# Kernel optimization log

Hardware: AMD Instinct MI355X
Metric: run time of the kernel (lower is better)

## Reference

```python
import jax, jax.numpy as jnp
import numpy as np

H, F, E_SHARED, E_ROUTED, K = 1024, 4096, 1, 8, 2


def setup_inputs() -> dict:
    key = jax.random.key(0)
    ks = jax.random.split(key, 6)
    x = jax.random.normal(ks[0], (4, 2048, H), dtype=jnp.float32)
    s = 0.02
    shared_up = jax.random.normal(ks[1], (E_SHARED, H, F), dtype=jnp.float32) * s
    shared_down = jax.random.normal(ks[2], (E_SHARED, F, H), dtype=jnp.float32) * s
    routed_up = jax.random.normal(ks[3], (E_ROUTED, H, F), dtype=jnp.float32) * s
    routed_down = jax.random.normal(ks[4], (E_ROUTED, F, H), dtype=jnp.float32) * s
    router_w = jax.random.normal(ks[5], (H, E_ROUTED), dtype=jnp.float32) * s
    return {"x": x, "shared_up": shared_up, "shared_down": shared_down,
            "routed_up": routed_up, "routed_down": routed_down, "router_w": router_w}


def _expert(x, w_up, w_down):
    # ExpertBlock: down(gelu(up(x))), exact (erf) gelu as in torch F.gelu default
    h = jax.nn.gelu(jnp.einsum('bsh,hf->bsf', x, w_up), approximate=False)
    return jnp.einsum('bsf,fh->bsh', h, w_down)


def reference(x, shared_up, shared_down, routed_up, routed_down, router_w):
    # shared experts (always active)
    shared_out = jnp.zeros_like(x)
    for i in range(E_SHARED):
        shared_out = shared_out + _expert(x, shared_up[i], shared_down[i])

    # router: softmax over routed experts, then top-k gating
    probs = jax.nn.softmax(jnp.einsum('bsh,he->bse', x, router_w), axis=-1)
    top_k_prob, top_k_idx = jax.lax.top_k(probs, K)  # [B,S,K]
    # per-expert gate = sum of top-k probs assigned to that expert
    onehot = jax.nn.one_hot(top_k_idx, E_ROUTED, dtype=x.dtype)  # [B,S,K,E]
    gates = jnp.einsum('bsk,bske->bse', top_k_prob, onehot)      # [B,S,E]

    routed_out = jnp.zeros_like(x)
    for e in range(E_ROUTED):  # fixed small loop over experts
        y = _expert(x, routed_up[e], routed_down[e])
        routed_out = routed_out + gates[..., e:e + 1] * y

    return shared_out + routed_out + x
```

## Files before the change

kernel.cpp:

```cpp
#include <hip/hip_runtime.h>
#include <cstdint>
#include <cstddef>

#define HD 1024
#define FF 4096
#define TOK 8192
#define NSEG 9
#define ROWS_ROUTED (TOK*2)
#define ROWS_TOT (ROWS_ROUTED + TOK)

typedef __bf16 bf16;
typedef __bf16 bf16x8 __attribute__((ext_vector_type(8)));
typedef float  f32x4  __attribute__((ext_vector_type(4)));

__device__ __forceinline__ void stage16(const void* g, void* l) {
  __builtin_amdgcn_global_load_lds((const __attribute__((address_space(1))) void*)g,
                                   (__attribute__((address_space(3))) void*)l,
                                   16, 0, 0);
}

__device__ __forceinline__ unsigned short bf_bits(float v) {
  bf16 b = (bf16)v;
  return __builtin_bit_cast(unsigned short, b);
}

__global__ void k_init_meta(int* meta) {
  int t = threadIdx.x;
  if (t < 64) meta[t] = 0;
}

__global__ void k_convert_x(const float* __restrict__ x, bf16* __restrict__ xbf) {
  int i = blockIdx.x*256 + threadIdx.x;
  float4 v = reinterpret_cast<const float4*>(x)[i];
  ushort4 u;
  u.x = bf_bits(v.x); u.y = bf_bits(v.y); u.z = bf_bits(v.z); u.w = bf_bits(v.w);
  reinterpret_cast<ushort4*>(xbf)[i] = u;
}

__global__ void k_copy_out(const float* __restrict__ x, float* __restrict__ out) {
  int i = blockIdx.x*256 + threadIdx.x;
  reinterpret_cast<float4*>(out)[i] = reinterpret_cast<const float4*>(x)[i];
}

__global__ void k_tcvt(const float* __restrict__ routed, const float* __restrict__ shared_,
                       bf16* __restrict__ dst, int R, int C) {
  int e = blockIdx.z;
  const float* src = (e < 8) ? (routed + (size_t)e*R*C) : shared_;
  bf16* d = dst + (size_t)e*R*C;
  __shared__ float lds[64][65];
  int r0 = blockIdx.y*64, c0 = blockIdx.x*64;
  int t = threadIdx.x;
  int tr = t>>4, tc4 = (t&15)*4;
  #pragma unroll
  for (int i=0;i<4;i++) {
    float4 v = *reinterpret_cast<const float4*>(src + (size_t)(r0+tr+i*16)*C + c0 + tc4);
    lds[tr+i*16][tc4+0]=v.x; lds[tr+i*16][tc4+1]=v.y;
    lds[tr+i*16][tc4+2]=v.z; lds[tr+i*16][tc4+3]=v.w;
  }
  __syncthreads();
  #pragma unroll
  for (int i=0;i<4;i++) {
    int oc = tr + i*16;
    ushort4 u;
    u.x = bf_bits(lds[tc4+0][oc]);
    u.y = bf_bits(lds[tc4+1][oc]);
    u.z = bf_bits(lds[tc4+2][oc]);
    u.w = bf_bits(lds[tc4+3][oc]);
    *reinterpret_cast<ushort4*>(d + (size_t)(c0+oc)*R + r0 + tc4) = u;
  }
}

__global__ void k_router(const float* __restrict__ x, const float* __restrict__ rw,
                         int* __restrict__ rtE, float* __restrict__ rtG,
                         int* __restrict__ meta) {
  __shared__ float rwl[HD*8];
  int t = threadIdx.x;
  for (int i=t;i<HD*8/4;i+=256)
    reinterpret_cast<float4*>(rwl)[i] = reinterpret_cast<const float4*>(rw)[i];
  __syncthreads();
  int wv = t>>6, lane = t&63;
  int tk = blockIdx.x*4 + wv;
  const float* xr = x + (size_t)tk*HD;
  float a[8] = {0,0,0,0,0,0,0,0};
  for (int i=0;i<HD/64;i++) {
    int h = lane + i*64;
    float xv = xr[h];
    const float* r = rwl + h*8;
    #pragma unroll
    for (int e=0;e<8;e++) a[e] = fmaf(xv, r[e], a[e]);
  }
  #pragma unroll
  for (int e=0;e<8;e++) {
    for (int s=32;s>0;s>>=1) a[e] += __shfl_xor(a[e], s, 64);
  }
  if (lane==0) {
    float mx = a[0];
    #pragma unroll
    for (int e=1;e<8;e++) mx = fmaxf(mx, a[e]);
    float p[8]; float den = 0.f;
    #pragma unroll
    for (int e=0;e<8;e++) { p[e] = expf(a[e]-mx); den += p[e]; }
    int i0 = 0;
    #pragma unroll
    for (int e=1;e<8;e++) if (p[e] > p[i0]) i0 = e;
    int i1 = (i0==0)?1:0;
    #pragma unroll
    for (int e=0;e<8;e++) if (e!=i0 && p[e] > p[i1]) i1 = e;
    float inv = 1.f/den;
    rtE[tk*2] = i0; rtE[tk*2+1] = i1;
    rtG[tk*2] = p[i0]*inv; rtG[tk*2+1] = p[i1]*inv;
    atomicAdd(&meta[i0], 1);
    atomicAdd(&meta[i1], 1);
  }
}

__global__ void k_prefix(int* meta) {
  if (threadIdx.x == 0) {
    int off = 0;
    for (int e=0;e<8;e++) { meta[16+e] = off; meta[32+e] = meta[e]; off += meta[e]; }
    meta[16+8] = ROWS_ROUTED;
    meta[32+8] = TOK;
  }
}

__global__ void k_scatter(const int* __restrict__ rtE, const float* __restrict__ rtG,
                          int* __restrict__ meta, int* __restrict__ tok,
                          float* __restrict__ gate) {
  int t = blockIdx.x*256 + threadIdx.x;
  int e0 = rtE[t*2], e1 = rtE[t*2+1];
  float g0 = rtG[t*2], g1 = rtG[t*2+1];
  int p0 = atomicAdd(&meta[8+e0], 1);
  int r0 = meta[16+e0] + p0;
  tok[r0] = t; gate[r0] = g0;
  int p1 = atomicAdd(&meta[8+e1], 1);
  int r1 = meta[16+e1] + p1;
  tok[r1] = t; gate[r1] = g1;
  tok[ROWS_ROUTED + t] = t; gate[ROWS_ROUTED + t] = 1.0f;
}


__global__ __launch_bounds__(256,2) void k_gemm_up(
    const bf16* __restrict__ xbf, const bf16* __restrict__ wupT,
    bf16* __restrict__ hbuf, const int* __restrict__ tok,
    const int* __restrict__ meta, int ch, int FC, int ntiles)
{
  int bx = blockIdx.x;
  int bps = 64*ntiles;
  int seg = bx / bps; int rem = bx % bps;
  int mt = rem / ntiles, nt = rem % ntiles;
  int rows = (seg<8)? meta[32+seg] : TOK;
  if (mt*128 >= rows) return;
  int segoff = meta[16+seg];
  int rowbase = mt*128;

  __shared__ __align__(16) bf16 Alds[128*32];
  __shared__ __align__(16) bf16 Blds[128*32];

  const int t = threadIdx.x;
  const int lane = t & 63, w = t >> 6;

  int lr0 = t>>2, lr1 = 64 + (t>>2);
  int gr0 = rowbase + lr0; if (gr0 >= rows) gr0 = rowbase;
  int gr1 = rowbase + lr1; if (gr1 >= rows) gr1 = rowbase;
  int tok0 = tok[segoff + gr0], tok1 = tok[segoff + gr1];
  int kswz = ((t&3) ^ ((t>>3)&3)) * 8;
  const bf16* gA0 = xbf + (size_t)tok0*HD + kswz;
  const bf16* gA1 = xbf + (size_t)tok1*HD + kswz;
  const bf16* wb = wupT + (size_t)seg*FF*HD;
  int f0 = ch*FC + nt*128;
  const bf16* gB0 = wb + (size_t)(f0 + lr0)*HD + kswz;
  const bf16* gB1 = wb + (size_t)(f0 + lr1)*HD + kswz;

  char* AldsB = (char*)Alds; char* BldsB = (char*)Blds;
  void* dstA0 = AldsB + w*1024;
  void* dstA1 = AldsB + 4096 + w*1024;
  void* dstB0 = BldsB + w*1024;
  void* dstB1 = BldsB + 4096 + w*1024;

  int slotb = ((lane>>4) ^ (((lane&15)>>1)&3)) * 16;
  const char* Abase = AldsB + ((w>>1)*64 + (lane&15))*64 + slotb;
  const char* Bbase = BldsB + ((w&1)*64 + (lane&15))*64 + slotb;

  f32x4 acc[4][4] = {};

  for (int k0=0; k0<HD; k0+=32) {
    stage16(gA0 + k0, dstA0);
    stage16(gA1 + k0, dstA1);
    stage16(gB0 + k0, dstB0);
    stage16(gB1 + k0, dstB1);
    __syncthreads();
    bf16x8 af[4], bfr[4];
    #pragma unroll
    for (int m=0;m<4;m++) af[m]  = *reinterpret_cast<const bf16x8*>(Abase + m*1024);
    #pragma unroll
    for (int n=0;n<4;n++) bfr[n] = *reinterpret_cast<const bf16x8*>(Bbase + n*1024);
    #pragma unroll
    for (int m=0;m<4;m++)
      #pragma unroll
      for (int n=0;n<4;n++)
        acc[m][n] = __builtin_amdgcn_mfma_f32_16x16x32_bf16(af[m], bfr[n], acc[m][n], 0,0,0);
    __syncthreads();
  }

  int lq = lane>>4, lrm = lane&15;
  #pragma unroll
  for (int m=0;m<4;m++) {
    #pragma unroll
    for (int n=0;n<4;n++) {
      #pragma unroll
      for (int j=0;j<4;j++) {
        int rl = (w>>1)*64 + m*16 + lq*4 + j;
        int gr = rowbase + rl;
        if (gr < rows) {
          float v = acc[m][n][j];
          v = 0.5f*v*(1.0f + erff(v*0.70710678118654752f));
          int cc = nt*128 + (w&1)*64 + n*16 + lrm;
          hbuf[(size_t)(segoff+gr)*FC + cc] = (bf16)v;
        }
      }
    }
  }
}

__global__ __launch_bounds__(256,2) void k_gemm_down(
    const bf16* __restrict__ hbuf, const bf16* __restrict__ wdnT,
    float* __restrict__ out, const int* __restrict__ tok, const float* __restrict__ gate,
    const int* __restrict__ meta, int ch, int FC)
{
  int bx = blockIdx.x;
  int seg = bx >> 9;
  int rem = bx & 511;
  int mt = rem >> 3, nt = rem & 7;
  int rows = (seg<8)? meta[32+seg] : TOK;
  if (mt*128 >= rows) return;
  int segoff = meta[16+seg];
  int rowbase = mt*128;

  __shared__ __align__(16) bf16 Alds[128*32];
  __shared__ __align__(16) bf16 Blds[128*32];
  __shared__ int tokL[128];
  __shared__ float gateL[128];

  const int t = threadIdx.x;
  const int lane = t & 63, w = t >> 6;

  if (t < 128) {
    int gr = rowbase + t; if (gr >= rows) gr = rows - 1;
    tokL[t] = tok[segoff + gr];
    gateL[t] = gate[segoff + gr];
  }

  int lr0 = t>>2, lr1 = 64 + (t>>2);
  int kswz = ((t&3) ^ ((t>>3)&3)) * 8;
  const bf16* gA0 = hbuf + (size_t)(segoff + rowbase + lr0)*FC + kswz;
  const bf16* gA1 = hbuf + (size_t)(segoff + rowbase + lr1)*FC + kswz;
  const bf16* wb = wdnT + (size_t)seg*HD*FF;
  int h0 = nt*128;
  const bf16* gB0 = wb + (size_t)(h0 + lr0)*FF + ch*FC + kswz;
  const bf16* gB1 = wb + (size_t)(h0 + lr1)*FF + ch*FC + kswz;

  char* AldsB = (char*)Alds; char* BldsB = (char*)Blds;
  void* dstA0 = AldsB + w*1024;
  void* dstA1 = AldsB + 4096 + w*1024;
  void* dstB0 = BldsB + w*1024;
  void* dstB1 = BldsB + 4096 + w*1024;

  int slotb = ((lane>>4) ^ (((lane&15)>>1)&3)) * 16;
  const char* Abase = AldsB + ((w>>1)*64 + (lane&15))*64 + slotb;
  const char* Bbase = BldsB + ((w&1)*64 + (lane&15))*64 + slotb;

  f32x4 acc[4][4] = {};

  for (int k0=0; k0<FC; k0+=32) {
    stage16(gA0 + k0, dstA0);
    stage16(gA1 + k0, dstA1);
    stage16(gB0 + k0, dstB0);
    stage16(gB1 + k0, dstB1);
    __syncthreads();
    bf16x8 af[4], bfr[4];
    #pragma unroll
    for (int m=0;m<4;m++) af[m]  = *reinterpret_cast<const bf16x8*>(Abase + m*1024);
    #pragma unroll
    for (int n=0;n<4;n++) bfr[n] = *reinterpret_cast<const bf16x8*>(Bbase + n*1024);
    #pragma unroll
    for (int m=0;m<4;m++)
      #pragma unroll
      for (int n=0;n<4;n++)
        acc[m][n] = __builtin_amdgcn_mfma_f32_16x16x32_bf16(af[m], bfr[n], acc[m][n], 0,0,0);
    __syncthreads();
  }

  int lq = lane>>4, lrm = lane&15;
  #pragma unroll
  for (int m=0;m<4;m++) {
    #pragma unroll
    for (int n=0;n<4;n++) {
      #pragma unroll
      for (int j=0;j<4;j++) {
        int rl = (w>>1)*64 + m*16 + lq*4 + j;
        int gr = rowbase + rl;
        if (gr < rows) {
          float v = acc[m][n][j] * gateL[rl];
          int cc = nt*128 + (w&1)*64 + n*16 + lrm;
          unsafeAtomicAdd(out + (size_t)tokL[rl]*HD + cc, v);
        }
      }
    }
  }
}

struct Layout {
  size_t xbf, wupT, wdnT, hbuf, tok, gate, rtE, rtG, meta, total;
};

static inline Layout make_layout(size_t FC) {
  Layout L; size_t o = 0;
  auto al = [&](size_t b){ o = (o+255)&~(size_t)255; size_t r=o; o+=b; return r; };
  L.xbf  = al((size_t)TOK*HD*2);
  L.wupT = al((size_t)NSEG*FF*HD*2);
  L.wdnT = al((size_t)NSEG*FF*HD*2);
  L.hbuf = al((size_t)ROWS_TOT*FC*2);
  L.tok  = al((size_t)ROWS_TOT*4);
  L.gate = al((size_t)ROWS_TOT*4);
  L.rtE  = al((size_t)TOK*2*4);
  L.rtG  = al((size_t)TOK*2*4);
  L.meta = al(256*4);
  L.total = o;
  return L;
}

extern "C" void kernel_launch(void* const* d_in, const int* in_sizes, int n_in,
                              void* d_out, int out_size, void* d_ws, size_t ws_size,
                              hipStream_t stream) {
  const float* x           = (const float*)d_in[0];
  const float* shared_up   = (const float*)d_in[1];
  const float* shared_down = (const float*)d_in[2];
  const float* routed_up   = (const float*)d_in[3];
  const float* routed_down = (const float*)d_in[4];
  const float* router_w    = (const float*)d_in[5];
  float* out = (float*)d_out;

  size_t FC = 2048;
  while (FC > 256 && make_layout(FC).total > ws_size) FC >>= 1;
  Layout L = make_layout(FC);

  char* ws = (char*)d_ws;
  bf16*  xbf  = (bf16*)(ws + L.xbf);
  bf16*  wupT = (bf16*)(ws + L.wupT);
  bf16*  wdnT = (bf16*)(ws + L.wdnT);
  bf16*  hbuf = (bf16*)(ws + L.hbuf);
  int*   tok  = (int*)(ws + L.tok);
  float* gate = (float*)(ws + L.gate);
  int*   rtE  = (int*)(ws + L.rtE);
  float* rtG  = (float*)(ws + L.rtG);
  int*   meta = (int*)(ws + L.meta);

  k_init_meta<<<1, 64, 0, stream>>>(meta);
  k_convert_x<<<TOK*HD/1024, 256, 0, stream>>>(x, xbf);
  k_tcvt<<<dim3(FF/64, HD/64, NSEG), 256, 0, stream>>>(routed_up, shared_up, wupT, HD, FF);
  k_tcvt<<<dim3(HD/64, FF/64, NSEG), 256, 0, stream>>>(routed_down, shared_down, wdnT, FF, HD);
  k_router<<<TOK/4, 256, 0, stream>>>(x, router_w, rtE, rtG, meta);
  k_prefix<<<1, 64, 0, stream>>>(meta);
  k_scatter<<<TOK/256, 256, 0, stream>>>(rtE, rtG, meta, tok, gate);
  k_copy_out<<<TOK*HD/1024, 256, 0, stream>>>(x, out);

  int ntiles = (int)(FC/128);
  int fc = (int)FC;
  for (int ch = 0; ch*fc < FF; ++ch) {
    k_gemm_up<<<NSEG*64*ntiles, 256, 0, stream>>>(xbf, wupT, hbuf, tok, meta, ch, fc, ntiles);
    k_gemm_down<<<NSEG*64*8, 256, 0, stream>>>(hbuf, wdnT, out, tok, gate, meta, ch, fc);
  }
}
```

Baseline: 1.099 ms.

## Double-buffer GEMM LDS, replace atomic scatter with bf16 buffer plus combine

Both expert GEMMs now double-buffer their LDS tiles, so the next K-slice loads while MFMAs run on the current one. MFMA operands are swapped so each lane holds contiguous columns, which lets the epilogue write packed bf16x4 vectors. The down GEMM no longer does fp32 atomic adds into the output. It writes gated per-row results to a bf16 buffer, and a new combine kernel sums x, the shared row and the two routed rows per token. FC is raised to 4096 to allow a single chunk, at the cost of extra workspace and bf16 rounding of the intermediate expert outputs.

Measured after the change: 1.044 ms. -5.1%, faster.

```diff
diff --git a/kernel.cpp b/kernel.cpp
--- a/kernel.cpp
+++ b/kernel.cpp
@@ -11,6 +11,7 @@
 
 typedef __bf16 bf16;
 typedef __bf16 bf16x8 __attribute__((ext_vector_type(8)));
+typedef __bf16 bf16x4 __attribute__((ext_vector_type(4)));
 typedef float  f32x4  __attribute__((ext_vector_type(4)));
 
 __device__ __forceinline__ void stage16(const void* g, void* l) {
@@ -35,11 +36,6 @@
   ushort4 u;
   u.x = bf_bits(v.x); u.y = bf_bits(v.y); u.z = bf_bits(v.z); u.w = bf_bits(v.w);
   reinterpret_cast<ushort4*>(xbf)[i] = u;
-}
-
-__global__ void k_copy_out(const float* __restrict__ x, float* __restrict__ out) {
-  int i = blockIdx.x*256 + threadIdx.x;
-  reinterpret_cast<float4*>(out)[i] = reinterpret_cast<const float4*>(x)[i];
 }
 
 __global__ void k_tcvt(const float* __restrict__ routed, const float* __restrict__ shared_,
@@ -125,17 +121,35 @@
 
 __global__ void k_scatter(const int* __restrict__ rtE, const float* __restrict__ rtG,
                           int* __restrict__ meta, int* __restrict__ tok,
-                          float* __restrict__ gate) {
+                          float* __restrict__ gate, int* __restrict__ trow) {
   int t = blockIdx.x*256 + threadIdx.x;
   int e0 = rtE[t*2], e1 = rtE[t*2+1];
   float g0 = rtG[t*2], g1 = rtG[t*2+1];
   int p0 = atomicAdd(&meta[8+e0], 1);
   int r0 = meta[16+e0] + p0;
-  tok[r0] = t; gate[r0] = g0;
+  tok[r0] = t; gate[r0] = g0; trow[t*2] = r0;
   int p1 = atomicAdd(&meta[8+e1], 1);
   int r1 = meta[16+e1] + p1;
-  tok[r1] = t; gate[r1] = g1;
+  tok[r1] = t; gate[r1] = g1; trow[t*2+1] = r1;
   tok[ROWS_ROUTED + t] = t; gate[ROWS_ROUTED + t] = 1.0f;
+}
+
+__global__ void k_combine(const float* __restrict__ x, const bf16* __restrict__ dbuf,
+                          const int* __restrict__ trow, float* __restrict__ out) {
+  int tkn = blockIdx.x;
+  int t = threadIdx.x;
+  int r0 = trow[tkn*2], r1 = trow[tkn*2+1];
+  int h = t*4;
+  float4 xv = *reinterpret_cast<const float4*>(x + (size_t)tkn*HD + h);
+  bf16x4 a = *reinterpret_cast<const bf16x4*>(dbuf + (size_t)(ROWS_ROUTED+tkn)*HD + h);
+  bf16x4 b = *reinterpret_cast<const bf16x4*>(dbuf + (size_t)r0*HD + h);
+  bf16x4 c = *reinterpret_cast<const bf16x4*>(dbuf + (size_t)r1*HD + h);
+  float4 o;
+  o.x = xv.x + (float)a[0] + (float)b[0] + (float)c[0];
+  o.y = xv.y + (float)a[1] + (float)b[1] + (float)c[1];
+  o.z = xv.z + (float)a[2] + (float)b[2] + (float)c[2];
+  o.w = xv.w + (float)a[3] + (float)b[3] + (float)c[3];
+  *reinterpret_cast<float4*>(out + (size_t)tkn*HD + h) = o;
 }
 
 
@@ -153,8 +167,8 @@
   int segoff = meta[16+seg];
   int rowbase = mt*128;
 
-  __shared__ __align__(16) bf16 Alds[128*32];
-  __shared__ __align__(16) bf16 Blds[128*32];
+  __shared__ __align__(16) bf16 Alds[2][128*32];
+  __shared__ __align__(16) bf16 Blds[2][128*32];
 
   const int t = threadIdx.x;
   const int lane = t & 63, w = t >> 6;
@@ -172,60 +186,83 @@
   const bf16* gB1 = wb + (size_t)(f0 + lr1)*HD + kswz;
 
   char* AldsB = (char*)Alds; char* BldsB = (char*)Blds;
-  void* dstA0 = AldsB + w*1024;
-  void* dstA1 = AldsB + 4096 + w*1024;
-  void* dstB0 = BldsB + w*1024;
-  void* dstB1 = BldsB + 4096 + w*1024;
-
-  int slotb = ((lane>>4) ^ (((lane&15)>>1)&3)) * 16;
-  const char* Abase = AldsB + ((w>>1)*64 + (lane&15))*64 + slotb;
-  const char* Bbase = BldsB + ((w&1)*64 + (lane&15))*64 + slotb;
+  const int stoff = w*1024;
+
+  const int slotb = ((lane>>4) ^ (((lane&15)>>1)&3)) * 16;
+  const int Afo = ((w>>1)*64 + (lane&15))*64 + slotb;
+  const int Bfo = ((w&1)*64 + (lane&15))*64 + slotb;
 
   f32x4 acc[4][4] = {};
 
-  for (int k0=0; k0<HD; k0+=32) {
-    stage16(gA0 + k0, dstA0);
-    stage16(gA1 + k0, dstA1);
-    stage16(gB0 + k0, dstB0);
-    stage16(gB1 + k0, dstB1);
-    __syncthreads();
+  stage16(gA0, AldsB + stoff);
+  stage16(gA1, AldsB + 4096 + stoff);
+  stage16(gB0, BldsB + stoff);
+  stage16(gB1, BldsB + 4096 + stoff);
+  __syncthreads();
+
+  int cur = 0;
+  for (int k0=32; k0<HD; k0+=32) {
+    char* an = AldsB + (cur^1)*8192;
+    char* bn = BldsB + (cur^1)*8192;
+    stage16(gA0 + k0, an + stoff);
+    stage16(gA1 + k0, an + 4096 + stoff);
+    stage16(gB0 + k0, bn + stoff);
+    stage16(gB1 + k0, bn + 4096 + stoff);
+    const char* Ab = AldsB + cur*8192 + Afo;
+    const char* Bb = BldsB + cur*8192 + Bfo;
     bf16x8 af[4], bfr[4];
     #pragma unroll
-    for (int m=0;m<4;m++) af[m]  = *reinterpret_cast<const bf16x8*>(Abase + m*1024);
-    #pragma unroll
-    for (int n=0;n<4;n++) bfr[n] = *reinterpret_cast<const bf16x8*>(Bbase + n*1024);
+    for (int m=0;m<4;m++) af[m]  = *reinterpret_cast<const bf16x8*>(Ab + m*1024);
+    #pragma unroll
+    for (int n=0;n<4;n++) bfr[n] = *reinterpret_cast<const bf16x8*>(Bb + n*1024);
     #pragma unroll
     for (int m=0;m<4;m++)
       #pragma unroll
       for (int n=0;n<4;n++)
-        acc[m][n] = __builtin_amdgcn_mfma_f32_16x16x32_bf16(af[m], bfr[n], acc[m][n], 0,0,0);
+        acc[m][n] = __builtin_amdgcn_mfma_f32_16x16x32_bf16(bfr[n], af[m], acc[m][n], 0,0,0);
     __syncthreads();
-  }
-
-  int lq = lane>>4, lrm = lane&15;
+    cur ^= 1;
+  }
+  {
+    const char* Ab = AldsB + cur*8192 + Afo;
+    const char* Bb = BldsB + cur*8192 + Bfo;
+    bf16x8 af[4], bfr[4];
+    #pragma unroll
+    for (int m=0;m<4;m++) af[m]  = *reinterpret_cast<const bf16x8*>(Ab + m*1024);
+    #pragma unroll
+    for (int n=0;n<4;n++) bfr[n] = *reinterpret_cast<const bf16x8*>(Bb + n*1024);
+    #pragma unroll
+    for (int m=0;m<4;m++)
+      #pragma unroll
+      for (int n=0;n<4;n++)
+        acc[m][n] = __builtin_amdgcn_mfma_f32_16x16x32_bf16(bfr[n], af[m], acc[m][n], 0,0,0);
+  }
+
+  const int lrm = lane&15, lq = lane>>4;
   #pragma unroll
   for (int m=0;m<4;m++) {
+    int rl = (w>>1)*64 + m*16 + lrm;
+    int gr = rowbase + rl;
+    if (gr >= rows) continue;
+    bf16* hrow = hbuf + (size_t)(segoff+gr)*FC + nt*128 + (w&1)*64 + lq*4;
     #pragma unroll
     for (int n=0;n<4;n++) {
+      bf16x4 u;
       #pragma unroll
       for (int j=0;j<4;j++) {
-        int rl = (w>>1)*64 + m*16 + lq*4 + j;
-        int gr = rowbase + rl;
-        if (gr < rows) {
-          float v = acc[m][n][j];
-          v = 0.5f*v*(1.0f + erff(v*0.70710678118654752f));
-          int cc = nt*128 + (w&1)*64 + n*16 + lrm;
-          hbuf[(size_t)(segoff+gr)*FC + cc] = (bf16)v;
-        }
+        float v = acc[m][n][j];
+        v = 0.5f*v*(1.0f + erff(v*0.70710678118654752f));
+        u[j] = (bf16)v;
       }
+      *reinterpret_cast<bf16x4*>(hrow + n*16) = u;
     }
   }
 }
 
 __global__ __launch_bounds__(256,2) void k_gemm_down(
     const bf16* __restrict__ hbuf, const bf16* __restrict__ wdnT,
-    float* __restrict__ out, const int* __restrict__ tok, const float* __restrict__ gate,
-    const int* __restrict__ meta, int ch, int FC)
+    bf16* __restrict__ dbuf, const float* __restrict__ gate,
+    const int* __restrict__ meta, int ch, int FC, int first)
 {
   int bx = blockIdx.x;
   int seg = bx >> 9;
@@ -236,9 +273,8 @@
   int segoff = meta[16+seg];
   int rowbase = mt*128;
 
-  __shared__ __align__(16) bf16 Alds[128*32];
-  __shared__ __align__(16) bf16 Blds[128*32];
-  __shared__ int tokL[128];
+  __shared__ __align__(16) bf16 Alds[2][128*32];
+  __shared__ __align__(16) bf16 Blds[2][128*32];
   __shared__ float gateL[128];
 
   const int t = threadIdx.x;
@@ -246,7 +282,6 @@
 
   if (t < 128) {
     int gr = rowbase + t; if (gr >= rows) gr = rows - 1;
-    tokL[t] = tok[segoff + gr];
     gateL[t] = gate[segoff + gr];
   }
 
@@ -260,57 +295,84 @@
   const bf16* gB1 = wb + (size_t)(h0 + lr1)*FF + ch*FC + kswz;
 
   char* AldsB = (char*)Alds; char* BldsB = (char*)Blds;
-  void* dstA0 = AldsB + w*1024;
-  void* dstA1 = AldsB + 4096 + w*1024;
-  void* dstB0 = BldsB + w*1024;
-  void* dstB1 = BldsB + 4096 + w*1024;
-
-  int slotb = ((lane>>4) ^ (((lane&15)>>1)&3)) * 16;
-  const char* Abase = AldsB + ((w>>1)*64 + (lane&15))*64 + slotb;
-  const char* Bbase = BldsB + ((w&1)*64 + (lane&15))*64 + slotb;
+  const int stoff = w*1024;
+
+  const int slotb = ((lane>>4) ^ (((lane&15)>>1)&3)) * 16;
+  const int Afo = ((w>>1)*64 + (lane&15))*64 + slotb;
+  const int Bfo = ((w&1)*64 + (lane&15))*64 + slotb;
 
   f32x4 acc[4][4] = {};
 
-  for (int k0=0; k0<FC; k0+=32) {
-    stage16(gA0 + k0, dstA0);
-    stage16(gA1 + k0, dstA1);
-    stage16(gB0 + k0, dstB0);
-    stage16(gB1 + k0, dstB1);
-    __syncthreads();
+  stage16(gA0, AldsB + stoff);
+  stage16(gA1, AldsB + 4096 + stoff);
+  stage16(gB0, BldsB + stoff);
+  stage16(gB1, BldsB + 4096 + stoff);
+  __syncthreads();
+
+  int cur = 0;
+  for (int k0=32; k0<FC; k0+=32) {
+    char* an = AldsB + (cur^1)*8192;
+    char* bn = BldsB + (cur^1)*8192;
+    stage16(gA0 + k0, an + stoff);
+    stage16(gA1 + k0, an + 4096 + stoff);
+    stage16(gB0 + k0, bn + stoff);
+    stage16(gB1 + k0, bn + 4096 + stoff);
+    const char* Ab = AldsB + cur*8192 + Afo;
+    const char* Bb = BldsB + cur*8192 + Bfo;
     bf16x8 af[4], bfr[4];
     #pragma unroll
-    for (int m=0;m<4;m++) af[m]  = *reinterpret_cast<const bf16x8*>(Abase + m*1024);
-    #pragma unroll
-    for (int n=0;n<4;n++) bfr[n] = *reinterpret_cast<const bf16x8*>(Bbase + n*1024);
+    for (int m=0;m<4;m++) af[m]  = *reinterpret_cast<const bf16x8*>(Ab + m*1024);
+    #pragma unroll
+    for (int n=0;n<4;n++) bfr[n] = *reinterpret_cast<const bf16x8*>(Bb + n*1024);
     #pragma unroll
     for (int m=0;m<4;m++)
       #pragma unroll
       for (int n=0;n<4;n++)
-        acc[m][n] = __builtin_amdgcn_mfma_f32_16x16x32_bf16(af[m], bfr[n], acc[m][n], 0,0,0);
+        acc[m][n] = __builtin_amdgcn_mfma_f32_16x16x32_bf16(bfr[n], af[m], acc[m][n], 0,0,0);
     __syncthreads();
-  }
-
-  int lq = lane>>4, lrm = lane&15;
+    cur ^= 1;
+  }
+  {
+    const char* Ab = AldsB + cur*8192 + Afo;
+    const char* Bb = BldsB + cur*8192 + Bfo;
+    bf16x8 af[4], bfr[4];
+    #pragma unroll
+    for (int m=0;m<4;m++) af[m]  = *reinterpret_cast<const bf16x8*>(Ab + m*1024);
+    #pragma unroll
+    for (int n=0;n<4;n++) bfr[n] = *reinterpret_cast<const bf16x8*>(Bb + n*1024);
+    #pragma unroll
+    for (int m=0;m<4;m++)
+      #pragma unroll
+      for (int n=0;n<4;n++)
+        acc[m][n] = __builtin_amdgcn_mfma_f32_16x16x32_bf16(bfr[n], af[m], acc[m][n], 0,0,0);
+  }
+
+  const int lrm = lane&15, lq = lane>>4;
   #pragma unroll
   for (int m=0;m<4;m++) {
+    int rl = (w>>1)*64 + m*16 + lrm;
+    int gr = rowbase + rl;
+    if (gr >= rows) continue;
+    float g = gateL[rl];
+    bf16* drow = dbuf + (size_t)(segoff+gr)*HD + nt*128 + (w&1)*64 + lq*4;
     #pragma unroll
     for (int n=0;n<4;n++) {
-      #pragma unroll
-      for (int j=0;j<4;j++) {
-        int rl = (w>>1)*64 + m*16 + lq*4 + j;
-        int gr = rowbase + rl;
-        if (gr < rows) {
-          float v = acc[m][n][j] * gateL[rl];
-          int cc = nt*128 + (w&1)*64 + n*16 + lrm;
-          unsafeAtomicAdd(out + (size_t)tokL[rl]*HD + cc, v);
-        }
+      bf16x4 u;
+      if (first) {
+        #pragma unroll
+        for (int j=0;j<4;j++) u[j] = (bf16)(acc[m][n][j]*g);
+      } else {
+        bf16x4 o = *reinterpret_cast<const bf16x4*>(drow + n*16);
+        #pragma unroll
+        for (int j=0;j<4;j++) u[j] = (bf16)((float)o[j] + acc[m][n][j]*g);
       }
+      *reinterpret_cast<bf16x4*>(drow + n*16) = u;
     }
   }
 }
 
 struct Layout {
-  size_t xbf, wupT, wdnT, hbuf, tok, gate, rtE, rtG, meta, total;
+  size_t xbf, wupT, wdnT, hbuf, dbuf, tok, gate, trow, rtE, rtG, meta, total;
 };
 
 static inline Layout make_layout(size_t FC) {
@@ -320,8 +382,10 @@
   L.wupT = al((size_t)NSEG*FF*HD*2);
   L.wdnT = al((size_t)NSEG*FF*HD*2);
   L.hbuf = al((size_t)ROWS_TOT*FC*2);
+  L.dbuf = al((size_t)ROWS_TOT*HD*2);
   L.tok  = al((size_t)ROWS_TOT*4);
   L.gate = al((size_t)ROWS_TOT*4);
+  L.trow = al((size_t)TOK*2*4);
   L.rtE  = al((size_t)TOK*2*4);
   L.rtG  = al((size_t)TOK*2*4);
   L.meta = al(256*4);
@@ -340,7 +404,7 @@
   const float* router_w    = (const float*)d_in[5];
   float* out = (float*)d_out;
 
-  size_t FC = 2048;
+  size_t FC = 4096;
   while (FC > 256 && make_layout(FC).total > ws_size) FC >>= 1;
   Layout L = make_layout(FC);
 
@@ -349,8 +413,10 @@
   bf16*  wupT = (bf16*)(ws + L.wupT);
   bf16*  wdnT = (bf16*)(ws + L.wdnT);
   bf16*  hbuf = (bf16*)(ws + L.hbuf);
+  bf16*  dbuf = (bf16*)(ws + L.dbuf);
   int*   tok  = (int*)(ws + L.tok);
   float* gate = (float*)(ws + L.gate);
+  int*   trow = (int*)(ws + L.trow);
   int*   rtE  = (int*)(ws + L.rtE);
   float* rtG  = (float*)(ws + L.rtG);
   int*   meta = (int*)(ws + L.meta);
@@ -361,13 +427,13 @@
   k_tcvt<<<dim3(HD/64, FF/64, NSEG), 256, 0, stream>>>(routed_down, shared_down, wdnT, FF, HD);
   k_router<<<TOK/4, 256, 0, stream>>>(x, router_w, rtE, rtG, meta);
   k_prefix<<<1, 64, 0, stream>>>(meta);
-  k_scatter<<<TOK/256, 256, 0, stream>>>(rtE, rtG, meta, tok, gate);
-  k_copy_out<<<TOK*HD/1024, 256, 0, stream>>>(x, out);
+  k_scatter<<<TOK/256, 256, 0, stream>>>(rtE, rtG, meta, tok, gate, trow);
 
   int ntiles = (int)(FC/128);
   int fc = (int)FC;
   for (int ch = 0; ch*fc < FF; ++ch) {
     k_gemm_up<<<NSEG*64*ntiles, 256, 0, stream>>>(xbf, wupT, hbuf, tok, meta, ch, fc, ntiles);
-    k_gemm_down<<<NSEG*64*8, 256, 0, stream>>>(hbuf, wdnT, out, tok, gate, meta, ch, fc);
-  }
-}
+    k_gemm_down<<<NSEG*64*8, 256, 0, stream>>>(hbuf, wdnT, dbuf, gate, meta, ch, fc, ch==0 ? 1 : 0);
+  }
+  k_combine<<<TOK, 256, 0, stream>>>(x, dbuf, trow, out);
+}
```
